# Performance work log

Measured on AMD Instinct MI355X. Metric: run time of the kernel, lower is better.

The kernel has to match this reference:

```python
import jax, jax.numpy as jnp
import numpy as np

D_MODEL = 1024
NUM_HEADS = 16
HEAD_DIM = D_MODEL // NUM_HEADS  # 64
ROPE_THETA = 10000.0
BATCH = 2
SEQ = 2048
NEG_INF = -1e30


def setup_inputs() -> dict:
    key = jax.random.key(0)
    ks = jax.random.split(key, 6)
    std = 1.0 / np.sqrt(D_MODEL)
    x = jax.random.normal(ks[0], (BATCH, SEQ, D_MODEL), dtype=jnp.float32)
    wq = jax.random.normal(ks[1], (D_MODEL, D_MODEL), dtype=jnp.float32) * std
    wk = jax.random.normal(ks[2], (D_MODEL, D_MODEL), dtype=jnp.float32) * std
    wv = jax.random.normal(ks[3], (D_MODEL, D_MODEL), dtype=jnp.float32) * std
    wo = jax.random.normal(ks[4], (D_MODEL, D_MODEL), dtype=jnp.float32) * std
    token_positions = jnp.broadcast_to(jnp.arange(SEQ, dtype=jnp.int32)[None, :], (BATCH, SEQ))
    return {"x": x, "token_positions": token_positions, "wq": wq, "wk": wk, "wv": wv, "wo": wo}


def _apply_rope(t, token_positions):
    # t: (B, H, S, head_dim), token_positions: (B, S)
    half = HEAD_DIM // 2
    inv_freq = 1.0 / (ROPE_THETA ** (2.0 * jnp.arange(half, dtype=jnp.float32) / HEAD_DIM))
    angles = token_positions.astype(jnp.float32)[..., None] * inv_freq  # (B, S, half)
    cos = jnp.cos(angles)[:, None, :, :]  # (B, 1, S, half)
    sin = jnp.sin(angles)[:, None, :, :]
    tp = t.reshape(*t.shape[:-1], half, 2)  # interleaved pairs
    x1, x2 = tp[..., 0], tp[..., 1]
    r1 = x1 * cos - x2 * sin
    r2 = x1 * sin + x2 * cos
    return jnp.stack([r1, r2], axis=-1).reshape(t.shape)


def reference(x, token_positions, wq, wk, wv, wo):
    B, S, D = x.shape
    H, hd = NUM_HEADS, HEAD_DIM
    # projections (Linear: y = x @ W.T, no bias)
    q = (x @ wq.T).reshape(B, S, H, hd).transpose(0, 2, 1, 3)  # (B, H, S, hd)
    k = (x @ wk.T).reshape(B, S, H, hd).transpose(0, 2, 1, 3)
    v = (x @ wv.T).reshape(B, S, H, hd).transpose(0, 2, 1, 3)
    # RoPE on Q, K
    q = _apply_rope(q, token_positions)
    k = _apply_rope(k, token_positions)
    # causal scaled dot-product attention
    scores = jnp.einsum("bhqd,bhkd->bhqk", q, k) / jnp.sqrt(jnp.float32(hd))
    mask = jnp.tril(jnp.ones((S, S), dtype=bool))
    scores = jnp.where(mask, scores, NEG_INF)
    probs = jax.nn.softmax(scores, axis=-1)
    attn = jnp.einsum("bhqk,bhkd->bhqd", probs, v)  # (B, H, S, hd)
    attn = attn.transpose(0, 2, 1, 3).reshape(B, S, D)
    return attn @ wo.T
```

## Files before the change

kernel.cpp:

```cpp
#include <hip/hip_runtime.h>
#include <stdint.h>
#include <math.h>

#define SEQ 2048
#define NH 16
#define DM 1024

typedef __bf16 bf16x8 __attribute__((ext_vector_type(8)));
typedef float f32x4 __attribute__((ext_vector_type(4)));

#define ASM_VMCNT0  asm volatile("s_waitcnt vmcnt(0)" ::: "memory")
#define ASM_BARRIER asm volatile("s_barrier" ::: "memory")

__device__ __forceinline__ unsigned short f2bf(float f) {
  union { float f; unsigned u; } v; v.f = f;
  unsigned r = v.u + 0x7fffu + ((v.u >> 16) & 1u);
  return (unsigned short)(r >> 16);
}
__device__ __forceinline__ unsigned pk2(float a, float b) {
  return (unsigned)f2bf(a) | ((unsigned)f2bf(b) << 16);
}
__device__ __forceinline__ void load_lds16(const void* g, void* l) {
  __builtin_amdgcn_global_load_lds((__attribute__((address_space(1))) void*)g,
                                   (__attribute__((address_space(3))) void*)l,
                                   16, 0, 0);
}

__global__ void cvt_all(const float* __restrict__ x, const float* __restrict__ wq,
                        const float* __restrict__ wk, const float* __restrict__ wv,
                        const float* __restrict__ wo, unsigned short* __restrict__ ws) {
  const int i = blockIdx.x * blockDim.x + threadIdx.x;
  const int off = i * 4;
  const float* src;
  unsigned short* dst;
  if (off < 4194304) {
    src = x + off;  dst = ws + off;
  } else {
    const int r = off - 4194304;
    const int w = r >> 20, o = r & 1048575;
    const float* tabs[4] = {wq, wk, wv, wo};
    src = tabs[w] + o;  dst = ws + 4194304 + (w << 20) + o;
  }
  const float4 v = *(const float4*)src;
  ushort4 u;
  u.x = f2bf(v.x); u.y = f2bf(v.y); u.z = f2bf(v.z); u.w = f2bf(v.w);
  *(ushort4*)dst = u;
}

__launch_bounds__(256, 2)
__global__ void gemm_qkv(const unsigned short* __restrict__ X,
                         const unsigned short* __restrict__ W3,
                         unsigned short* __restrict__ Qr,
                         unsigned short* __restrict__ Kr,
                         unsigned short* __restrict__ Vt,
                         const int* __restrict__ tp) {
  __shared__ __align__(16) char smem[32768];

  const int t = threadIdx.x;
  const int lane = t & 63, wave = t >> 6;
  const int quad = lane >> 4, l16 = lane & 15;
  const int m0 = blockIdx.y * 128, n0 = blockIdx.x * 128;
  const int wm = (wave >> 1) * 64, wn = (wave & 1) * 64;

  f32x4 acc[4][4];
#pragma unroll
  for (int i = 0; i < 4; i++)
#pragma unroll
    for (int j = 0; j < 4; j++) { acc[i][j][0]=0.f; acc[i][j][1]=0.f; acc[i][j][2]=0.f; acc[i][j][3]=0.f; }

  const int rr = t >> 2;
  const int cc = (t & 3) * 8;

#define QKV_STAGE(bufidx, k0_) do {                                               \
    char* a_ = smem + (bufidx) * 8192;                                            \
    char* b_ = smem + 16384 + (bufidx) * 8192;                                    \
    _Pragma("unroll")                                                             \
    for (int i_ = 0; i_ < 2; i_++) {                                              \
      load_lds16(X  + (uint64_t)(m0 + i_ * 64 + rr) * 1024 + (k0_) + cc,          \
                 a_ + i_ * 4096 + wave * 1024);                                   \
      load_lds16(W3 + (uint64_t)(n0 + i_ * 64 + rr) * 1024 + (k0_) + cc,          \
                 b_ + i_ * 4096 + wave * 1024);                                   \
    }                                                                             \
  } while (0)

  QKV_STAGE(0, 0);

  for (int k0 = 0; k0 < 1024; k0 += 32) {
    const int buf = (k0 >> 5) & 1;
    ASM_VMCNT0;
    ASM_BARRIER;
    if (k0 + 32 < 1024) QKV_STAGE(buf ^ 1, k0 + 32);
    char* As = smem + buf * 8192;
    char* Bs = smem + 16384 + buf * 8192;

    bf16x8 af[4], bfr[4];
#pragma unroll
    for (int i = 0; i < 4; i++) {
      af[i]  = *(const bf16x8*)(As + (wm + i * 16 + l16) * 64 + quad * 16);
      bfr[i] = *(const bf16x8*)(Bs + (wn + i * 16 + l16) * 64 + quad * 16);
    }
#pragma unroll
    for (int i = 0; i < 4; i++)
#pragma unroll
      for (int j = 0; j < 4; j++)
        acc[i][j] = __builtin_amdgcn_mfma_f32_16x16x32_bf16(af[i], bfr[j], acc[i][j], 0, 0, 0);
  }
#undef QKV_STAGE

  if (n0 < 2048) {
    unsigned short* dst = (n0 < 1024) ? Qr : Kr;
    float fr[4]; int dd[4], hh[4];
#pragma unroll
    for (int j = 0; j < 4; j++) {
      const int n = n0 + wn + j * 16 + l16;
      dd[j] = n & 63;
      hh[j] = (n & 1023) >> 6;
      fr[j] = __builtin_amdgcn_exp2f(-0.20762050594f * (float)(dd[j] & ~1)) * 0.15915494309f;
    }
    const float sgnodd = (l16 & 1) ? 1.f : -1.f;
#pragma unroll
    for (int i = 0; i < 4; i++) {
#pragma unroll
      for (int r = 0; r < 4; r++) {
        const int m = m0 + wm + i * 16 + quad * 4 + r;
        const int s = m & 2047, b = m >> 11;
        const float posf = (float)tp[m];
#pragma unroll
        for (int j = 0; j < 4; j++) {
          const float v = acc[i][j][r];
          const float p = __shfl_xor(v, 1);
          float rev = posf * fr[j];
          rev -= floorf(rev);
          float sn, cs;
          asm("v_sin_f32 %0, %1" : "=v"(sn) : "v"(rev));
          asm("v_cos_f32 %0, %1" : "=v"(cs) : "v"(rev));
          const float rv = fmaf(v, cs, p * sn * sgnodd);
          dst[((uint64_t)((b * NH + hh[j]) * SEQ + s)) * 64 + dd[j]] = f2bf(rv);
        }
      }
    }
  } else {
#pragma unroll
    for (int i = 0; i < 4; i++) {
      const int m = m0 + wm + i * 16 + quad * 4;
      const int s = m & 2047, b = m >> 11;
#pragma unroll
      for (int j = 0; j < 4; j++) {
        const int n = n0 - 2048 + wn + j * 16 + l16;
        const int h = n >> 6, d = n & 63;
        uint2 w;
        w.x = pk2(acc[i][j][0], acc[i][j][1]);
        w.y = pk2(acc[i][j][2], acc[i][j][3]);
        *(uint2*)(Vt + ((uint64_t)((b * NH + h) * 64 + d)) * SEQ + s) = w;
      }
    }
  }
}

__launch_bounds__(256, 2)
__global__ void gemm_ao(const unsigned short* __restrict__ A,
                        const unsigned short* __restrict__ B,
                        float* __restrict__ C) {
  __shared__ __align__(16) char smem[24576];

  const int t = threadIdx.x;
  const int lane = t & 63, wave = t >> 6;
  const int quad = lane >> 4, l16 = lane & 15;
  const int m0 = blockIdx.y * 128, n0 = blockIdx.x * 64;
  const int wm = (wave >> 1) * 64, wn = (wave & 1) * 32;

  f32x4 acc[4][2];
#pragma unroll
  for (int i = 0; i < 4; i++)
#pragma unroll
    for (int j = 0; j < 2; j++) { acc[i][j][0]=0.f; acc[i][j][1]=0.f; acc[i][j][2]=0.f; acc[i][j][3]=0.f; }

  const int rr = t >> 2;
  const int cc = (t & 3) * 8;

#define AO_STAGE(bufidx, k0_) do {                                                \
    char* a_ = smem + (bufidx) * 8192;                                            \
    char* b_ = smem + 16384 + (bufidx) * 4096;                                    \
    _Pragma("unroll")                                                             \
    for (int i_ = 0; i_ < 2; i_++)                                                \
      load_lds16(A + (uint64_t)(m0 + i_ * 64 + rr) * 1024 + (k0_) + cc,           \
                 a_ + i_ * 4096 + wave * 1024);                                   \
    load_lds16(B + (uint64_t)(n0 + rr) * 1024 + (k0_) + cc, b_ + wave * 1024);    \
  } while (0)

  AO_STAGE(0, 0);

  for (int k0 = 0; k0 < 1024; k0 += 32) {
    const int buf = (k0 >> 5) & 1;
    ASM_VMCNT0;
    ASM_BARRIER;
    if (k0 + 32 < 1024) AO_STAGE(buf ^ 1, k0 + 32);
    char* As = smem + buf * 8192;
    char* Bs = smem + 16384 + buf * 4096;

    bf16x8 af[4], bfr[2];
#pragma unroll
    for (int i = 0; i < 4; i++)
      af[i] = *(const bf16x8*)(As + (wm + i * 16 + l16) * 64 + quad * 16);
#pragma unroll
    for (int j = 0; j < 2; j++)
      bfr[j] = *(const bf16x8*)(Bs + (wn + j * 16 + l16) * 64 + quad * 16);
#pragma unroll
    for (int i = 0; i < 4; i++)
#pragma unroll
      for (int j = 0; j < 2; j++)
        acc[i][j] = __builtin_amdgcn_mfma_f32_16x16x32_bf16(af[i], bfr[j], acc[i][j], 0, 0, 0);
  }
#undef AO_STAGE

#pragma unroll
  for (int i = 0; i < 4; i++)
#pragma unroll
    for (int j = 0; j < 2; j++)
#pragma unroll
      for (int r = 0; r < 4; r++) {
        const int m = m0 + wm + i * 16 + quad * 4 + r;
        const int n = n0 + wn + j * 16 + l16;
        C[(uint64_t)m * DM + n] = acc[i][j][r];
      }
}

__launch_bounds__(256, 4)
__global__ void flash_attn(const unsigned short* __restrict__ Q,
                           const unsigned short* __restrict__ K,
                           const unsigned short* __restrict__ Vt,
                           unsigned short* __restrict__ Oa) {
  __shared__ __align__(16) char smem[40960];

  const int t = threadIdx.x;
  const int lane = t & 63, wave = t >> 6;
  const int quad = lane >> 4, l16 = lane & 15;
  const int bx = blockIdx.x;
  const int qt = (bx & 1) ? (31 - (bx >> 1)) : (bx >> 1);
  const int bh = blockIdx.y;
  const int qbase = qt * 64;
  const uint64_t base = (uint64_t)bh * (SEQ * 64);
  const int qg = qbase + wave * 16 + l16;

  bf16x8 qf[2];
  {
    const unsigned short* qp = Q + base + (uint64_t)qg * 64 + quad * 8;
    qf[0] = *(const bf16x8*)qp;
    qf[1] = *(const bf16x8*)(qp + 32);
  }

  f32x4 o[4];
#pragma unroll
  for (int i = 0; i < 4; i++) { o[i][0]=0.f; o[i][1]=0.f; o[i][2]=0.f; o[i][3]=0.f; }
  float mI = -1e30f, lI = 0.f;

  const int srow = wave * 8 + (lane >> 3);
  const int sc = ((lane & 7) ^ (lane >> 3)) * 8;
  const int swz = (l16 & 7);
  char* ps = smem + 32768 + wave * 2048;

#define STAGE(bufidx, kb_) do {                                                   \
    char* kd_ = smem + (bufidx) * 8192;                                           \
    char* vd_ = smem + 16384 + (bufidx) * 8192;                                   \
    _Pragma("unroll")                                                             \
    for (int i_ = 0; i_ < 2; i_++) {                                              \
      load_lds16(K  + base + (uint64_t)((kb_) + i_ * 32 + srow) * 64 + sc,        \
                 kd_ + i_ * 4096 + wave * 1024);                                  \
      load_lds16(Vt + base + (uint64_t)(i_ * 32 + srow) * SEQ + (kb_) + sc,       \
                 vd_ + i_ * 4096 + wave * 1024);                                  \
    }                                                                             \
  } while (0)

  STAGE(0, 0);

  for (int kt = 0; kt <= qt; kt++) {
    const int kb = kt * 64;
    const int buf = kt & 1;
    ASM_VMCNT0;
    ASM_BARRIER;
    if (kt < qt) STAGE(buf ^ 1, kb + 64);
    char* ks = smem + buf * 8192;
    char* vs = smem + 16384 + buf * 8192;
    const bool diag = (kt == qt);
    const int nbmax = diag ? (wave + 1) : 4;

    f32x4 sf[4];
#pragma unroll
    for (int nb = 0; nb < 4; nb++) {
      if (nb < nbmax) {
        f32x4 s; s[0]=0.f; s[1]=0.f; s[2]=0.f; s[3]=0.f;
#pragma unroll
        for (int kk = 0; kk < 2; kk++) {
          bf16x8 kfr = *(const bf16x8*)(ks + (nb * 16 + l16) * 128 + (((kk * 4 + quad) ^ swz) * 16));
          s = __builtin_amdgcn_mfma_f32_16x16x32_bf16(kfr, qf[kk], s, 0, 0, 0);
        }
        sf[nb] = s;
      } else {
        sf[nb][0] = -1e30f; sf[nb][1] = -1e30f; sf[nb][2] = -1e30f; sf[nb][3] = -1e30f;
      }
    }
    if (diag) {
#pragma unroll
      for (int nb = 0; nb < 4; nb++)
#pragma unroll
        for (int r = 0; r < 4; r++)
          if (kb + nb * 16 + quad * 4 + r > qg) sf[nb][r] = -1e30f;
    }

    float mx = sf[0][0];
#pragma unroll
    for (int nb = 0; nb < 4; nb++)
#pragma unroll
      for (int r = 0; r < 4; r++) mx = fmaxf(mx, sf[nb][r]);
    mx = fmaxf(mx, __shfl_xor(mx, 16));
    mx = fmaxf(mx, __shfl_xor(mx, 32));
    const float mnew = fmaxf(mI, mx);
    const float c1 = 0.18033688011f;
    const float mc = mnew * c1;
    const float alpha = __builtin_amdgcn_exp2f(mI * c1 - mc);
    mI = mnew;
    float ls = 0.f;
#pragma unroll
    for (int nb = 0; nb < 4; nb++)
#pragma unroll
      for (int r = 0; r < 4; r++) {
        const float p = __builtin_amdgcn_exp2f(sf[nb][r] * c1 - mc);
        sf[nb][r] = p;
        ls += p;
      }
    lI = lI * alpha + ls;
#pragma unroll
    for (int db = 0; db < 4; db++)
#pragma unroll
      for (int r = 0; r < 4; r++) o[db][r] *= alpha;

#pragma unroll
    for (int nb = 0; nb < 4; nb++) {
      uint2 pv;
      pv.x = pk2(sf[nb][0], sf[nb][1]);
      pv.y = pk2(sf[nb][2], sf[nb][3]);
      *(uint2*)(ps + l16 * 128 + (((nb * 2 + (quad >> 1)) ^ swz) * 16) + (quad & 1) * 8) = pv;
    }

    const int kkmax = diag ? ((wave >> 1) + 1) : 2;
    for (int kk = 0; kk < kkmax; kk++) {
      bf16x8 pf = *(const bf16x8*)(ps + l16 * 128 + (((kk * 4 + quad) ^ swz) * 16));
#pragma unroll
      for (int db = 0; db < 4; db++) {
        bf16x8 vf = *(const bf16x8*)(vs + (db * 16 + l16) * 128 + (((kk * 4 + quad) ^ swz) * 16));
        o[db] = __builtin_amdgcn_mfma_f32_16x16x32_bf16(vf, pf, o[db], 0, 0, 0);
      }
    }
  }
#undef STAGE

  lI += __shfl_xor(lI, 16);
  lI += __shfl_xor(lI, 32);
  const float invl = 1.0f / lI;
  const int b = bh >> 4, h = bh & 15;
  unsigned short* orow = Oa + ((uint64_t)(b * SEQ + qg)) * DM + h * 64 + quad * 4;
#pragma unroll
  for (int db = 0; db < 4; db++) {
    uint2 w;
    w.x = pk2(o[db][0] * invl, o[db][1] * invl);
    w.y = pk2(o[db][2] * invl, o[db][3] * invl);
    *(uint2*)(orow + db * 16) = w;
  }
}

extern "C" void kernel_launch(void* const* d_in, const int* in_sizes, int n_in,
                              void* d_out, int out_size, void* d_ws, size_t ws_size,
                              hipStream_t stream) {
  const float* x  = (const float*)d_in[0];
  const int* tp   = (const int*)d_in[1];
  const float* wq = (const float*)d_in[2];
  const float* wk = (const float*)d_in[3];
  const float* wv = (const float*)d_in[4];
  const float* wo = (const float*)d_in[5];
  float* out = (float*)d_out;

  unsigned short* ws = (unsigned short*)d_ws;
  unsigned short* xb  = ws;
  unsigned short* w3b = ws + 4194304;
  unsigned short* wob = ws + 7340032;
  unsigned short* Qr  = ws + 8388608;
  unsigned short* Kr  = ws + 12582912;
  unsigned short* Vt  = ws + 16777216;
  unsigned short* At  = ws + 20971520;

  cvt_all<<<8192, 256, 0, stream>>>(x, wq, wk, wv, wo, ws);
  gemm_qkv<<<dim3(24, 32), 256, 0, stream>>>(xb, w3b, Qr, Kr, Vt, tp);
  flash_attn<<<dim3(32, 32), 256, 0, stream>>>(Qr, Kr, Vt, At);
  gemm_ao<<<dim3(16, 32), 256, 0, stream>>>(At, wob, out);
}
```

Before: 207.0 us.

## Use hardware bf16 pack conversion and remap flash-attention blocks for load balance

```diff
diff --git a/kernel.cpp b/kernel.cpp
--- a/kernel.cpp
+++ b/kernel.cpp
@@ -7,7 +7,9 @@
 #define DM 1024
 
 typedef __bf16 bf16x8 __attribute__((ext_vector_type(8)));
+typedef __bf16 bf16x2 __attribute__((ext_vector_type(2)));
 typedef float f32x4 __attribute__((ext_vector_type(4)));
+typedef float f32x2 __attribute__((ext_vector_type(2)));
 
 #define ASM_VMCNT0  asm volatile("s_waitcnt vmcnt(0)" ::: "memory")
 #define ASM_BARRIER asm volatile("s_barrier" ::: "memory")
@@ -18,7 +20,10 @@
   return (unsigned short)(r >> 16);
 }
 __device__ __forceinline__ unsigned pk2(float a, float b) {
-  return (unsigned)f2bf(a) | ((unsigned)f2bf(b) << 16);
+  f32x2 v = {a, b};
+  bf16x2 r = __builtin_convertvector(v, bf16x2);
+  union { bf16x2 h; unsigned u; } c; c.h = r;
+  return c.u;
 }
 __device__ __forceinline__ void load_lds16(const void* g, void* l) {
   __builtin_amdgcn_global_load_lds((__attribute__((address_space(1))) void*)g,
@@ -42,9 +47,10 @@
     src = tabs[w] + o;  dst = ws + 4194304 + (w << 20) + o;
   }
   const float4 v = *(const float4*)src;
-  ushort4 u;
-  u.x = f2bf(v.x); u.y = f2bf(v.y); u.z = f2bf(v.z); u.w = f2bf(v.w);
-  *(ushort4*)dst = u;
+  uint2 u;
+  u.x = pk2(v.x, v.y);
+  u.y = pk2(v.z, v.w);
+  *(uint2*)dst = u;
 }
 
 __launch_bounds__(256, 2)
@@ -235,9 +241,12 @@
   const int t = threadIdx.x;
   const int lane = t & 63, wave = t >> 6;
   const int quad = lane >> 4, l16 = lane & 15;
-  const int bx = blockIdx.x;
-  const int qt = (bx & 1) ? (31 - (bx >> 1)) : (bx >> 1);
-  const int bh = blockIdx.y;
+  const int lid = blockIdx.x;
+  const int bh = lid & 31;
+  const int j = lid >> 5;
+  const int a = j & 7, p = j >> 3;
+  const int pb = (p >> 1) << 4;
+  const int qt = (p & 1) ? (pb + 15 - a) : (pb + a);
   const int qbase = qt * 64;
   const uint64_t base = (uint64_t)bh * (SEQ * 64);
   const int qg = qbase + wave * 16 + l16;
@@ -324,9 +333,9 @@
     for (int nb = 0; nb < 4; nb++)
 #pragma unroll
       for (int r = 0; r < 4; r++) {
-        const float p = __builtin_amdgcn_exp2f(sf[nb][r] * c1 - mc);
-        sf[nb][r] = p;
-        ls += p;
+        const float p2 = __builtin_amdgcn_exp2f(sf[nb][r] * c1 - mc);
+        sf[nb][r] = p2;
+        ls += p2;
       }
     lI = lI * alpha + ls;
 #pragma unroll
@@ -390,6 +399,6 @@
 
   cvt_all<<<8192, 256, 0, stream>>>(x, wq, wk, wv, wo, ws);
   gemm_qkv<<<dim3(24, 32), 256, 0, stream>>>(xb, w3b, Qr, Kr, Vt, tp);
-  flash_attn<<<dim3(32, 32), 256, 0, stream>>>(Qr, Kr, Vt, At);
+  flash_attn<<<1024, 256, 0, stream>>>(Qr, Kr, Vt, At);
   gemm_ao<<<dim3(16, 32), 256, 0, stream>>>(At, wob, out);
 }
```

New measurement: 181.9 us. 1.14x faster.
